# Kernel optimization log

Measured on AMD Instinct MI355X. Metric: run time of the kernel, lower is better.

Reference implementation:

```python
import jax, jax.numpy as jnp
import numpy as np

N_NODES = 100000
N_EDGES = 1600000
N_REL = 8
IN_CH = 64
HIDDEN = 64
OUT_CH = 32


def setup_inputs() -> dict:
    key = jax.random.key(0)
    ks = jax.random.split(key, 10)
    s_in = 1.0 / np.sqrt(IN_CH)
    s_h = 1.0 / np.sqrt(HIDDEN)
    return {
        "x": jax.random.normal(ks[0], (N_NODES, IN_CH), dtype=jnp.float32),
        "edge_index": jax.random.randint(ks[1], (2, N_EDGES), 0, N_NODES, dtype=jnp.int64),
        "edge_type": jax.random.randint(ks[2], (N_EDGES,), 0, N_REL, dtype=jnp.int64),
        "W0": jax.random.normal(ks[3], (N_REL, IN_CH, HIDDEN), dtype=jnp.float32) * s_in,
        "Q0": jax.random.normal(ks[4], (HIDDEN, 1), dtype=jnp.float32) * s_h,
        "K0": jax.random.normal(ks[5], (HIDDEN, 1), dtype=jnp.float32) * s_h,
        "b0": jnp.zeros((HIDDEN,), dtype=jnp.float32),
        "W1": jax.random.normal(ks[6], (N_REL, HIDDEN, OUT_CH), dtype=jnp.float32) * s_h,
        "Q1": jax.random.normal(ks[7], (OUT_CH, 1), dtype=jnp.float32) * (1.0 / np.sqrt(OUT_CH)),
        "K1": jax.random.normal(ks[8], (OUT_CH, 1), dtype=jnp.float32) * (1.0 / np.sqrt(OUT_CH)),
        "b1": jnp.zeros((OUT_CH,), dtype=jnp.float32),
    }


def rgat_conv(x, src, dst, et, W, Q, K, b, n_nodes):
    # relation-typed transform of all nodes: [R, N, out]
    xw = jnp.einsum("ni,rio->rno", x, W)
    # per-node, per-relation attention logits (heads=1, dim=1)
    q = jnp.einsum("rno,od->rnd", xw, Q)[..., 0]  # [R, N]
    k = jnp.einsum("rno,od->rnd", xw, K)[..., 0]  # [R, N]
    # additive self-attention, leaky_relu slope 0.2 (PyG RGATConv default)
    alpha = jax.nn.leaky_relu(q[et, dst] + k[et, src], negative_slope=0.2)  # [E]
    # across-relation segment softmax over incoming edges of each dst node
    amax = jax.ops.segment_max(alpha, dst, num_segments=n_nodes)
    a = jnp.exp(alpha - amax[dst])
    denom = jax.ops.segment_sum(a, dst, num_segments=n_nodes)
    a = a / (denom[dst] + 1e-16)
    # weighted scatter-add aggregation of transformed source features
    msg = a[:, None] * xw[et, src]  # [E, out]
    return jax.ops.segment_sum(msg, dst, num_segments=n_nodes) + b


def reference(x, edge_index, edge_type, W0, Q0, K0, b0, W1, Q1, K1, b1):
    src, dst = edge_index[0], edge_index[1]
    n = x.shape[0]
    h = rgat_conv(x, src, dst, edge_type, W0, Q0, K0, b0, n)
    h = jax.nn.relu(h)  # dropout p=0.0 -> identity
    out = rgat_conv(h, src, dst, edge_type, W1, Q1, K1, b1, n)
    return out
```

## Files before the change

kernel.cpp:

```cpp
#include <hip/hip_runtime.h>
#include <hip/hip_bf16.h>
#include <math.h>


#define CSR_CHUNK 8192

__global__ void k_bhist(const int* __restrict__ dst, int* __restrict__ bcount,
                        int E, int NB) {
    __shared__ int h[512];
    int t = threadIdx.x;
    for (int i = t; i < NB; i += 256) h[i] = 0;
    __syncthreads();
    int e0 = blockIdx.x * CSR_CHUNK;
    int e1 = min(e0 + CSR_CHUNK, E);
    for (int i = e0 + t; i < e1; i += 256) atomicAdd(&h[dst[i] >> 8], 1);
    __syncthreads();
    for (int i = t; i < NB; i += 256) {
        int c = h[i];
        if (c) atomicAdd(&bcount[i], c);
    }
}

__global__ void k_bscan(const int* __restrict__ bcount, int* __restrict__ bstart,
                        int* __restrict__ gcur, int* __restrict__ rowptr,
                        int NB, int N, int E) {
    __shared__ int s[512];
    int t = threadIdx.x;
    int v = (t < NB) ? bcount[t] : 0;
    s[t] = v;
    __syncthreads();
    for (int off = 1; off < 512; off <<= 1) {
        int a = (t >= off) ? s[t - off] : 0;
        __syncthreads();
        s[t] += a;
        __syncthreads();
    }
    int excl = s[t] - v;
    if (t < NB) {
        bstart[t] = excl;
        gcur[t] = excl;
    }
    if (t == 0) {
        bstart[NB] = E;
        rowptr[N] = E;
    }
}

__global__ void k_bscatter(const int* __restrict__ src, const int* __restrict__ dst,
                           const int* __restrict__ et, int* __restrict__ gcur,
                           unsigned* __restrict__ ebuf, int E, int NB) {
    __shared__ int h[512];
    __shared__ int basearr[512];
    int t = threadIdx.x;
    for (int i = t; i < NB; i += 256) h[i] = 0;
    __syncthreads();
    int e0 = blockIdx.x * CSR_CHUNK;
    int e1 = min(e0 + CSR_CHUNK, E);
    for (int i = e0 + t; i < e1; i += 256) atomicAdd(&h[dst[i] >> 8], 1);
    __syncthreads();
    for (int i = t; i < NB; i += 256) {
        int c = h[i];
        basearr[i] = c ? atomicAdd(&gcur[i], c) : 0;
        h[i] = 0;
    }
    __syncthreads();
    for (int i = e0 + t; i < e1; i += 256) {
        int d = dst[i];
        int b = d >> 8;
        int off = atomicAdd(&h[b], 1);
        ebuf[basearr[b] + off] =
            ((unsigned)(d & 255) << 20) | ((unsigned)et[i] << 17) | (unsigned)src[i];
    }
}

__global__ void k_bsort(const unsigned* __restrict__ ebuf, const int* __restrict__ bstart,
                        int* __restrict__ rowptr, int* __restrict__ csr, int N) {
    __shared__ int lh[2048];
    __shared__ int ls[2048];
    __shared__ int ss[256];
    int b = blockIdx.x, t = threadIdx.x;
    int e0 = bstart[b], e1 = bstart[b + 1];
    for (int i = t; i < 2048; i += 256) lh[i] = 0;
    __syncthreads();
    for (int i = e0 + t; i < e1; i += 256) {
        unsigned u = ebuf[i];
        atomicAdd(&lh[(int)(((u >> 20) & 255) * 8 + ((u >> 17) & 7))], 1);
    }
    __syncthreads();
    int loc[8];
    int s = 0;
#pragma unroll
    for (int j = 0; j < 8; j++) {
        loc[j] = s;
        s += lh[t * 8 + j];
    }
    ss[t] = s;
    __syncthreads();
    for (int off = 1; off < 256; off <<= 1) {
        int a = (t >= off) ? ss[t - off] : 0;
        __syncthreads();
        ss[t] += a;
        __syncthreads();
    }
    int excl = ss[t] - s;
#pragma unroll
    for (int j = 0; j < 8; j++) ls[t * 8 + j] = excl + loc[j];
    int node = b * 256 + t;
    if (node < N) rowptr[node] = e0 + excl;
    __syncthreads();
    for (int i = t; i < 2048; i += 256) lh[i] = 0;
    __syncthreads();
    for (int i = e0 + t; i < e1; i += 256) {
        unsigned u = ebuf[i];
        int key = (int)(((u >> 20) & 255) * 8 + ((u >> 17) & 7));
        int off = atomicAdd(&lh[key], 1);
        csr[e0 + ls[key] + off] = (int)u;
    }
}


__global__ void k_wt2(const float* __restrict__ W, __hip_bfloat16* __restrict__ hi,
                      __hip_bfloat16* __restrict__ lo, int OUT, int total) {
    int t = blockIdx.x * blockDim.x + threadIdx.x;
    if (t < total) {
        int per = 64 * OUT;
        int r = t / per;
        int rem = t % per;
        int i = rem / OUT;
        int o = rem % OUT;
        float v = W[t];
        __hip_bfloat16 h = __float2bfloat16(v);
        __hip_bfloat16 l = __float2bfloat16(v - __bfloat162float(h));
        size_t idx = (size_t)o * 512 + i * 8 + r;
        hi[idx] = h;
        lo[idx] = l;
    }
}

__global__ void k_wqk(const float* W, const float* Qv, const float* Kv,
                      float* wq, float* wk, int OUT) {
    int t = blockIdx.x * blockDim.x + threadIdx.x;
    if (t < 8 * 64) {
        int r = t >> 6, i = t & 63;
        const float* wrow = W + ((size_t)r * 64 + i) * OUT;
        float a = 0.f, b = 0.f;
        for (int o = 0; o < OUT; o++) {
            float w = wrow[o];
            a += w * Qv[o];
            b += w * Kv[o];
        }
        wq[t] = a;
        wk[t] = b;
    }
}

__global__ __launch_bounds__(256) void k_qk2(
        const float* __restrict__ xin, const float* __restrict__ wq,
        const float* __restrict__ wk, float* __restrict__ qn,
        float* __restrict__ kn, unsigned short* __restrict__ xbb, int N) {
    __shared__ float xt[64][65];
    __shared__ float swq[8 * 65], swk[8 * 65];
    int t = threadIdx.x;
    int nb0 = blockIdx.x * 64;
    for (int i = t; i < 512; i += 256) {
        int r = i >> 6, c = i & 63;
        swq[r * 65 + c] = wq[i];
        swk[r * 65 + c] = wk[i];
    }
    for (int i = t; i < 1024; i += 256) {
        int ns = i >> 4;
        int c4 = i & 15;
        int n = nb0 + ns;
        float4 v = {0.f, 0.f, 0.f, 0.f};
        if (n < N) v = ((const float4*)xin)[(size_t)n * 16 + c4];
        xt[ns][c4 * 4 + 0] = v.x;
        xt[ns][c4 * 4 + 1] = v.y;
        xt[ns][c4 * 4 + 2] = v.z;
        xt[ns][c4 * 4 + 3] = v.w;
        if (n < N) {
            __hip_bfloat16 b0 = __float2bfloat16(v.x);
            __hip_bfloat16 b1 = __float2bfloat16(v.y);
            __hip_bfloat16 b2 = __float2bfloat16(v.z);
            __hip_bfloat16 b3 = __float2bfloat16(v.w);
            ushort4 o;
            o.x = *(unsigned short*)&b0;
            o.y = *(unsigned short*)&b1;
            o.z = *(unsigned short*)&b2;
            o.w = *(unsigned short*)&b3;
            *(ushort4*)(xbb + (size_t)n * 64 + c4 * 4) = o;
        }
    }
    __syncthreads();
#pragma unroll
    for (int g = t; g < 512; g += 256) {
        int ns = g >> 3, r = g & 7;
        int n = nb0 + ns;
        if (n < N) {
            float qa = 0.f, ka = 0.f;
#pragma unroll
            for (int i = 0; i < 64; i++) {
                float xv = xt[ns][i];
                qa += xv * swq[r * 65 + i];
                ka += xv * swk[r * 65 + i];
            }
            qn[(size_t)n * 8 + r] = qa;
            kn[(size_t)n * 8 + r] = ka;
        }
    }
}

#define ZSTR 520

#define FLUSH8()                          \
    do {                                  \
        switch (currel) {                 \
            case 0: a0 += racc; break;    \
            case 1: a1 += racc; break;    \
            case 2: a2 += racc; break;    \
            case 3: a3 += racc; break;    \
            case 4: a4 += racc; break;    \
            case 5: a5 += racc; break;    \
            case 6: a6 += racc; break;    \
            case 7: a7 += racc; break;    \
        }                                 \
    } while (0)

template <int OUT, bool RELU>
__global__ __launch_bounds__(256) void k_fused(
        const int* __restrict__ rowptr, const int* __restrict__ csr,
        const float* __restrict__ qn, const float* __restrict__ kn,
        const unsigned short* __restrict__ xb,
        const __hip_bfloat16* __restrict__ wthi,
        const __hip_bfloat16* __restrict__ wtlo,
        const float* __restrict__ bias, float* __restrict__ xout, int N) {
    using v8s = __attribute__((ext_vector_type(8))) short;
    using v4f = __attribute__((ext_vector_type(4))) float;
    __shared__ unsigned short zt[16 * ZSTR];
    int t = threadIdx.x;
    int wvu = __builtin_amdgcn_readfirstlane(t >> 6);
    int lane = t & 63;
    int nb0 = blockIdx.x * 16;

    {
        uint4 zz = {0u, 0u, 0u, 0u};
#pragma unroll
        for (int q = 0; q < 4; q++)
            *(uint4*)&zt[(wvu * 4 + q) * ZSTR + lane * 8] = zz;
    }

#pragma unroll 1
    for (int q = 0; q < 4; q++) {
        int wid = nb0 + wvu * 4 + q;
        if (wid >= N) break;
        int r0 = rowptr[wid];
        int r1 = rowptr[wid + 1];
        int qvec = 0;
        if (lane < 8) qvec = ((const int*)qn)[wid * 8 + lane];

        float a0 = 0.f, a1 = 0.f, a2 = 0.f, a3 = 0.f;
        float a4 = 0.f, a5 = 0.f, a6 = 0.f, a7 = 0.f;
        float racc = 0.f, denom = 0.f;
        int currel = 0;

#pragma unroll 1
        for (int j = r0; j < r1; j += 16) {
            int pk[16];
            float kv[16];
            unsigned short xu[16];
#pragma unroll
            for (int u = 0; u < 16; u++) {
                int ii = (j + u < r1) ? (j + u) : (r1 - 1);
                pk[u] = csr[ii];
            }
#pragma unroll
            for (int u = 0; u < 16; u++) {
                int s_ = pk[u] & 0x1FFFF;
                int r_ = (pk[u] >> 17) & 7;
                kv[u] = kn[(size_t)s_ * 8 + r_];
            }
#pragma unroll
            for (int u = 0; u < 16; u++)
                xu[u] = xb[(size_t)(pk[u] & 0x1FFFF) * 64 + lane];
#pragma unroll
            for (int u = 0; u < 16; u++) {
                int rl = (pk[u] >> 17) & 7;
                float qv = __uint_as_float(__builtin_amdgcn_readlane(qvec, rl));
                float v = qv + kv[u];
                v = fmaxf(v, 0.2f * v);
                float tv = __expf(v);
                if (j + u >= r1) tv = 0.f;
                if (rl != currel) {
                    FLUSH8();
                    currel = rl;
                    racc = 0.f;
                }
                racc += tv * __uint_as_float(((unsigned)xu[u]) << 16);
                denom += tv;
            }
        }
        FLUSH8();
        float inv = 1.f / (denom + 1e-16f);
        float av[8] = {a0, a1, a2, a3, a4, a5, a6, a7};
        unsigned short us[8];
#pragma unroll
        for (int r = 0; r < 8; r++) {
            __hip_bfloat16 b = __float2bfloat16(av[r] * inv);
            us[r] = *(unsigned short*)&b;
        }
        uint4 pack;
        pack.x = (unsigned)us[0] | ((unsigned)us[1] << 16);
        pack.y = (unsigned)us[2] | ((unsigned)us[3] << 16);
        pack.z = (unsigned)us[4] | ((unsigned)us[5] << 16);
        pack.w = (unsigned)us[6] | ((unsigned)us[7] << 16);
        *(uint4*)&zt[(wvu * 4 + q) * ZSTR + lane * 8] = pack;
    }
    __syncthreads();

    int quad = lane >> 4;
    int l15 = lane & 15;
    int nt = wvu;
    if (nt * 16 < OUT) {
        const short* wh = (const short*)wthi;
        const short* wl = (const short*)wtlo;
        v4f acc = {0.f, 0.f, 0.f, 0.f};
#pragma unroll
        for (int k0 = 0; k0 < 512; k0 += 32) {
            int koff = k0 + quad * 8;
            v8s A = *(const v8s*)&zt[l15 * ZSTR + koff];
            v8s bh = *(const v8s*)(wh + (size_t)(nt * 16 + l15) * 512 + koff);
            v8s bl = *(const v8s*)(wl + (size_t)(nt * 16 + l15) * 512 + koff);
            acc = __builtin_amdgcn_mfma_f32_16x16x32_bf16(A, bh, acc, 0, 0, 0);
            acc = __builtin_amdgcn_mfma_f32_16x16x32_bf16(A, bl, acc, 0, 0, 0);
        }
        float bcol = bias[nt * 16 + l15];
#pragma unroll
        for (int g = 0; g < 4; g++) {
            int row = nb0 + quad * 4 + g;
            if (row < N) {
                float o = acc[g] + bcol;
                if (RELU) o = fmaxf(o, 0.f);
                xout[(size_t)row * OUT + nt * 16 + l15] = o;
            }
        }
    }
}


extern "C" void kernel_launch(void* const* d_in, const int* in_sizes, int n_in,
                              void* d_out, int out_size, void* d_ws, size_t ws_size,
                              hipStream_t stream) {
    const float* x   = (const float*)d_in[0];
    const int*   ei  = (const int*)d_in[1];
    const int*   et  = (const int*)d_in[2];
    const float* W0  = (const float*)d_in[3];
    const float* Q0  = (const float*)d_in[4];
    const float* K0  = (const float*)d_in[5];
    const float* b0  = (const float*)d_in[6];
    const float* W1  = (const float*)d_in[7];
    const float* Q1  = (const float*)d_in[8];
    const float* K1  = (const float*)d_in[9];
    const float* b1  = (const float*)d_in[10];
    float* out = (float*)d_out;

    const int N = in_sizes[0] / 64;
    const int E = in_sizes[2];
    const int* src = ei;
    const int* dst = ei + E;
    const int NB = (N + 255) >> 8;

    char* p = (char*)d_ws;
    auto alloc = [&](size_t bytes) -> void* {
        void* r = (void*)p;
        p += ((bytes + 255) / 256) * 256;
        return r;
    };
    int* rowptr   = (int*)alloc((size_t)(N + 1) * 4);
    int* bcount   = (int*)alloc(513 * 4);
    int* bstart   = (int*)alloc(513 * 4);
    int* gcur     = (int*)alloc(513 * 4);
    unsigned* ebuf = (unsigned*)alloc((size_t)E * 4);
    int* csr      = (int*)alloc((size_t)E * 4);
    float* wq     = (float*)alloc(8 * 64 * 4);
    float* wk     = (float*)alloc(8 * 64 * 4);
    float* qn     = (float*)alloc((size_t)N * 8 * 4);
    float* kn     = (float*)alloc((size_t)N * 8 * 4);
    __hip_bfloat16* wthi = (__hip_bfloat16*)alloc((size_t)64 * 512 * 2);
    __hip_bfloat16* wtlo = (__hip_bfloat16*)alloc((size_t)64 * 512 * 2);
    float* h      = (float*)alloc((size_t)N * 64 * 4);
    unsigned short* xbb = (unsigned short*)alloc((size_t)N * 64 * 2);

    int nchunks = (E + CSR_CHUNK - 1) / CSR_CHUNK;
    hipMemsetAsync(bcount, 0, (size_t)NB * 4, stream);
    k_bhist<<<nchunks, 256, 0, stream>>>(dst, bcount, E, NB);
    k_bscan<<<1, 512, 0, stream>>>(bcount, bstart, gcur, rowptr, NB, N, E);
    k_bscatter<<<nchunks, 256, 0, stream>>>(src, dst, et, gcur, ebuf, E, NB);
    k_bsort<<<NB, 256, 0, stream>>>(ebuf, bstart, rowptr, csr, N);

    int nfb = (N + 15) / 16;
    int nqkb = (N + 63) / 64;

    k_wqk<<<2, 256, 0, stream>>>(W0, Q0, K0, wq, wk, 64);
    k_qk2<<<nqkb, 256, 0, stream>>>(x, wq, wk, qn, kn, xbb, N);
    k_wt2<<<(8 * 64 * 64 + 255) / 256, 256, 0, stream>>>(W0, wthi, wtlo, 64, 8 * 64 * 64);
    k_fused<64, true><<<nfb, 256, 0, stream>>>(rowptr, csr, qn, kn, xbb,
                                               wthi, wtlo, b0, h, N);

    k_wqk<<<2, 256, 0, stream>>>(W1, Q1, K1, wq, wk, 32);
    k_qk2<<<nqkb, 256, 0, stream>>>(h, wq, wk, qn, kn, xbb, N);
    k_wt2<<<(8 * 64 * 32 + 255) / 256, 256, 0, stream>>>(W1, wthi, wtlo, 32, 8 * 64 * 32);
    k_fused<32, false><<<nfb, 256, 0, stream>>>(rowptr, csr, qn, kn, xbb,
                                                wthi, wtlo, b1, out, N);
}
```

Baseline: 474.3 us.

## Pre-gather source features into dst-sorted edge message buffer via src-bucketed scatter

Adds a second bucketing of edges by source node. A new kernel reads each source node's bf16 features from shared memory and writes them into a per-edge message array laid out in dst-CSR order. A separate attention kernel computes the exp-logits and inverse denominators per dst bucket. The fused aggregation then streams messages contiguously instead of doing random gathers of source rows. This turns random reads into scattered writes of an E×64 bf16 buffer (about 200MB) plus extra sort passes, which adds a lot of memory traffic in exchange for coalesced reads.

New measurement: 484.9 us. 1.02x slower.

```diff
diff --git a/kernel.cpp b/kernel.cpp
--- a/kernel.cpp
+++ b/kernel.cpp
@@ -5,25 +5,33 @@
 
 #define CSR_CHUNK 8192
 
-__global__ void k_bhist(const int* __restrict__ dst, int* __restrict__ bcount,
+__global__ void k_bhist(const int* __restrict__ dst, const int* __restrict__ src,
+                        int* __restrict__ bcount, int* __restrict__ sbcount,
                         int E, int NB) {
     __shared__ int h[512];
-    int t = threadIdx.x;
-    for (int i = t; i < NB; i += 256) h[i] = 0;
+    __shared__ int h2[512];
+    int t = threadIdx.x;
+    for (int i = t; i < NB; i += 256) { h[i] = 0; h2[i] = 0; }
     __syncthreads();
     int e0 = blockIdx.x * CSR_CHUNK;
     int e1 = min(e0 + CSR_CHUNK, E);
-    for (int i = e0 + t; i < e1; i += 256) atomicAdd(&h[dst[i] >> 8], 1);
+    for (int i = e0 + t; i < e1; i += 256) {
+        atomicAdd(&h[dst[i] >> 8], 1);
+        atomicAdd(&h2[src[i] >> 8], 1);
+    }
     __syncthreads();
     for (int i = t; i < NB; i += 256) {
         int c = h[i];
         if (c) atomicAdd(&bcount[i], c);
+        int c2 = h2[i];
+        if (c2) atomicAdd(&sbcount[i], c2);
     }
 }
 
 __global__ void k_bscan(const int* __restrict__ bcount, int* __restrict__ bstart,
                         int* __restrict__ gcur, int* __restrict__ rowptr,
-                        int NB, int N, int E) {
+                        const int* __restrict__ sbcount, int* __restrict__ sbstart,
+                        int* __restrict__ sgcur, int NB, int N, int E) {
     __shared__ int s[512];
     int t = threadIdx.x;
     int v = (t < NB) ? bcount[t] : 0;
@@ -36,19 +44,27 @@
         __syncthreads();
     }
     int excl = s[t] - v;
-    if (t < NB) {
-        bstart[t] = excl;
-        gcur[t] = excl;
-    }
-    if (t == 0) {
-        bstart[NB] = E;
-        rowptr[N] = E;
-    }
+    if (t < NB) { bstart[t] = excl; gcur[t] = excl; }
+    if (t == 0) { bstart[NB] = E; rowptr[N] = E; }
+    __syncthreads();
+    int v2 = (t < NB) ? sbcount[t] : 0;
+    s[t] = v2;
+    __syncthreads();
+    for (int off = 1; off < 512; off <<= 1) {
+        int a = (t >= off) ? s[t - off] : 0;
+        __syncthreads();
+        s[t] += a;
+        __syncthreads();
+    }
+    int excl2 = s[t] - v2;
+    if (t < NB) { sbstart[t] = excl2; sgcur[t] = excl2; }
+    if (t == 0) sbstart[NB] = E;
 }
 
 __global__ void k_bscatter(const int* __restrict__ src, const int* __restrict__ dst,
                            const int* __restrict__ et, int* __restrict__ gcur,
-                           unsigned* __restrict__ ebuf, int E, int NB) {
+                           unsigned* __restrict__ ebufA, int* __restrict__ ebufE,
+                           int E, int NB) {
     __shared__ int h[512];
     __shared__ int basearr[512];
     int t = threadIdx.x;
@@ -68,13 +84,16 @@
         int d = dst[i];
         int b = d >> 8;
         int off = atomicAdd(&h[b], 1);
-        ebuf[basearr[b] + off] =
-            ((unsigned)(d & 255) << 20) | ((unsigned)et[i] << 17) | (unsigned)src[i];
-    }
-}
-
-__global__ void k_bsort(const unsigned* __restrict__ ebuf, const int* __restrict__ bstart,
-                        int* __restrict__ rowptr, int* __restrict__ csr, int N) {
+        int pos = basearr[b] + off;
+        ebufA[pos] = ((unsigned)(d & 255) << 20) | ((unsigned)et[i] << 17) | (unsigned)src[i];
+        ebufE[pos] = i;
+    }
+}
+
+__global__ void k_bsort(const unsigned* __restrict__ ebufA, const int* __restrict__ ebufE,
+                        const int* __restrict__ bstart, int* __restrict__ rowptr,
+                        int* __restrict__ csr_pk, unsigned short* __restrict__ csr2,
+                        int* __restrict__ eidpos, int N) {
     __shared__ int lh[2048];
     __shared__ int ls[2048];
     __shared__ int ss[256];
@@ -83,7 +102,7 @@
     for (int i = t; i < 2048; i += 256) lh[i] = 0;
     __syncthreads();
     for (int i = e0 + t; i < e1; i += 256) {
-        unsigned u = ebuf[i];
+        unsigned u = ebufA[i];
         atomicAdd(&lh[(int)(((u >> 20) & 255) * 8 + ((u >> 17) & 7))], 1);
     }
     __syncthreads();
@@ -111,10 +130,40 @@
     for (int i = t; i < 2048; i += 256) lh[i] = 0;
     __syncthreads();
     for (int i = e0 + t; i < e1; i += 256) {
-        unsigned u = ebuf[i];
+        unsigned u = ebufA[i];
         int key = (int)(((u >> 20) & 255) * 8 + ((u >> 17) & 7));
         int off = atomicAdd(&lh[key], 1);
-        csr[e0 + ls[key] + off] = (int)u;
+        int cpos = e0 + ls[key] + off;
+        csr_pk[cpos] = (int)u;
+        csr2[cpos] = (unsigned short)((((u >> 20) & 255) << 3) | ((u >> 17) & 7));
+        if (eidpos) eidpos[ebufE[i]] = cpos;
+    }
+}
+
+__global__ void k_bscatter2(const int* __restrict__ src, const int* __restrict__ et,
+                            const int* __restrict__ eidpos, int* __restrict__ sgcur,
+                            unsigned* __restrict__ srcb, int E, int NB) {
+    __shared__ int h[512];
+    __shared__ int basearr[512];
+    int t = threadIdx.x;
+    for (int i = t; i < NB; i += 256) h[i] = 0;
+    __syncthreads();
+    int e0 = blockIdx.x * CSR_CHUNK;
+    int e1 = min(e0 + CSR_CHUNK, E);
+    for (int i = e0 + t; i < e1; i += 256) atomicAdd(&h[src[i] >> 8], 1);
+    __syncthreads();
+    for (int i = t; i < NB; i += 256) {
+        int c = h[i];
+        basearr[i] = c ? atomicAdd(&sgcur[i], c) : 0;
+        h[i] = 0;
+    }
+    __syncthreads();
+    for (int i = e0 + t; i < e1; i += 256) {
+        int sv = src[i];
+        int b = sv >> 8;
+        int off = atomicAdd(&h[b], 1);
+        srcb[basearr[b] + off] = ((unsigned)(sv & 255) << 24) |
+                                 ((unsigned)et[i] << 21) | (unsigned)eidpos[i];
     }
 }
 
@@ -209,6 +258,74 @@
     }
 }
 
+__global__ __launch_bounds__(256) void k_msg(
+        const unsigned* __restrict__ srcb, const int* __restrict__ sbstart,
+        const unsigned short* __restrict__ xbb, const float* __restrict__ kn,
+        unsigned short* __restrict__ msg, float* __restrict__ kvarr, int N) {
+    __shared__ unsigned short xrow[256 * 64];
+    __shared__ float knl[256 * 8];
+    int t = threadIdx.x;
+    int wv = t >> 6;
+    int lane = t & 63;
+    int b = blockIdx.x >> 2;
+    int qq = blockIdx.x & 3;
+    int nb = b * 256;
+    for (int idx = t; idx < 8192; idx += 256) {
+        int node = nb + (idx >> 5);
+        ((unsigned*)xrow)[idx] =
+            (node < N) ? ((const unsigned*)xbb)[(size_t)node * 32 + (idx & 31)] : 0u;
+    }
+    for (int idx = t; idx < 2048; idx += 256) {
+        int node = nb + (idx >> 3);
+        knl[idx] = (node < N) ? kn[(size_t)node * 8 + (idx & 7)] : 0.f;
+    }
+    __syncthreads();
+    int sb0 = sbstart[b], sb1 = sbstart[b + 1];
+    int len = sb1 - sb0;
+    int q0 = sb0 + ((len * qq) >> 2);
+    int q1 = sb0 + ((len * (qq + 1)) >> 2);
+    for (int i = q0 + wv; i < q1; i += 4) {
+        unsigned rec = (unsigned)__builtin_amdgcn_readfirstlane((int)srcb[i]);
+        int srcl = rec >> 24;
+        int rel = (rec >> 21) & 7;
+        int cp = rec & 0x1FFFFF;
+        unsigned short xv = xrow[srcl * 64 + lane];
+        msg[(size_t)cp * 64 + lane] = xv;
+        if (lane == 0) kvarr[cp] = knl[srcl * 8 + rel];
+    }
+}
+
+__global__ __launch_bounds__(256) void k_att(
+        const unsigned short* __restrict__ csr2, const float* __restrict__ kvarr,
+        const float* __restrict__ qn, const int* __restrict__ bstart,
+        float* __restrict__ tva, float* __restrict__ invden, int N) {
+    __shared__ float sq[2048];
+    __shared__ float sden[256];
+    int t = threadIdx.x;
+    int b = blockIdx.x;
+    int nb = b * 256;
+    for (int idx = t; idx < 2048; idx += 256) {
+        int node = nb + (idx >> 3);
+        sq[idx] = (node < N) ? qn[(size_t)node * 8 + (idx & 7)] : 0.f;
+    }
+    sden[t] = 0.f;
+    __syncthreads();
+    int e0 = bstart[b], e1 = bstart[b + 1];
+    for (int e = e0 + t; e < e1; e += 256) {
+        int c2 = csr2[e];
+        int dl = c2 >> 3;
+        int rel = c2 & 7;
+        float v = sq[dl * 8 + rel] + kvarr[e];
+        v = fmaxf(v, 0.2f * v);
+        float tvv = __expf(v);
+        tva[e] = tvv;
+        atomicAdd(&sden[dl], tvv);
+    }
+    __syncthreads();
+    int node = nb + t;
+    if (node < N) invden[node] = 1.f / (sden[t] + 1e-16f);
+}
+
 #define ZSTR 520
 
 #define FLUSH8()                          \
@@ -226,6 +343,113 @@
     } while (0)
 
 template <int OUT, bool RELU>
+__global__ __launch_bounds__(256) void k_fused2(
+        const int* __restrict__ rowptr, const unsigned short* __restrict__ csr2,
+        const float* __restrict__ tva, const float* __restrict__ invden,
+        const unsigned short* __restrict__ msg,
+        const __hip_bfloat16* __restrict__ wthi,
+        const __hip_bfloat16* __restrict__ wtlo,
+        const float* __restrict__ bias, float* __restrict__ xout, int N) {
+    using v8s = __attribute__((ext_vector_type(8))) short;
+    using v4f = __attribute__((ext_vector_type(4))) float;
+    __shared__ unsigned short zt[16 * ZSTR];
+    int t = threadIdx.x;
+    int wvu = __builtin_amdgcn_readfirstlane(t >> 6);
+    int lane = t & 63;
+    int nb0 = blockIdx.x * 16;
+
+    {
+        uint4 zz = {0u, 0u, 0u, 0u};
+#pragma unroll
+        for (int q = 0; q < 4; q++)
+            *(uint4*)&zt[(wvu * 4 + q) * ZSTR + lane * 8] = zz;
+    }
+
+#pragma unroll 1
+    for (int q = 0; q < 4; q++) {
+        int wid = nb0 + wvu * 4 + q;
+        if (wid >= N) break;
+        int r0 = rowptr[wid];
+        int r1 = rowptr[wid + 1];
+        float a0 = 0.f, a1 = 0.f, a2 = 0.f, a3 = 0.f;
+        float a4 = 0.f, a5 = 0.f, a6 = 0.f, a7 = 0.f;
+        float racc = 0.f;
+        int currel = 0;
+#pragma unroll 1
+        for (int j = r0; j < r1; j += 16) {
+            int c2[16];
+            float tvv[16];
+            unsigned short xu[16];
+#pragma unroll
+            for (int u = 0; u < 16; u++) {
+                int ii = (j + u < r1) ? (j + u) : (r1 - 1);
+                c2[u] = csr2[ii];
+                tvv[u] = (j + u < r1) ? tva[ii] : 0.f;
+            }
+#pragma unroll
+            for (int u = 0; u < 16; u++) {
+                int ii = (j + u < r1) ? (j + u) : (r1 - 1);
+                xu[u] = msg[(size_t)ii * 64 + lane];
+            }
+#pragma unroll
+            for (int u = 0; u < 16; u++) {
+                int rl = c2[u] & 7;
+                if (rl != currel) {
+                    FLUSH8();
+                    currel = rl;
+                    racc = 0.f;
+                }
+                racc += tvv[u] * __uint_as_float(((unsigned)xu[u]) << 16);
+            }
+        }
+        FLUSH8();
+        float inv = invden[wid];
+        float av[8] = {a0, a1, a2, a3, a4, a5, a6, a7};
+        unsigned short us[8];
+#pragma unroll
+        for (int r = 0; r < 8; r++) {
+            __hip_bfloat16 b = __float2bfloat16(av[r] * inv);
+            us[r] = *(unsigned short*)&b;
+        }
+        uint4 pack;
+        pack.x = (unsigned)us[0] | ((unsigned)us[1] << 16);
+        pack.y = (unsigned)us[2] | ((unsigned)us[3] << 16);
+        pack.z = (unsigned)us[4] | ((unsigned)us[5] << 16);
+        pack.w = (unsigned)us[6] | ((unsigned)us[7] << 16);
+        *(uint4*)&zt[(wvu * 4 + q) * ZSTR + lane * 8] = pack;
+    }
+    __syncthreads();
+
+    int quad = lane >> 4;
+    int l15 = lane & 15;
+    int nt = wvu;
+    if (nt * 16 < OUT) {
+        const short* wh = (const short*)wthi;
+        const short* wl = (const short*)wtlo;
+        v4f acc = {0.f, 0.f, 0.f, 0.f};
+#pragma unroll
+        for (int k0 = 0; k0 < 512; k0 += 32) {
+            int koff = k0 + quad * 8;
+            v8s A = *(const v8s*)&zt[l15 * ZSTR + koff];
+            v8s bh = *(const v8s*)(wh + (size_t)(nt * 16 + l15) * 512 + koff);
+            v8s bl = *(const v8s*)(wl + (size_t)(nt * 16 + l15) * 512 + koff);
+            acc = __builtin_amdgcn_mfma_f32_16x16x32_bf16(A, bh, acc, 0, 0, 0);
+            acc = __builtin_amdgcn_mfma_f32_16x16x32_bf16(A, bl, acc, 0, 0, 0);
+        }
+        float bcol = bias[nt * 16 + l15];
+#pragma unroll
+        for (int g = 0; g < 4; g++) {
+            int row = nb0 + quad * 4 + g;
+            if (row < N) {
+                float o = acc[g] + bcol;
+                if (RELU) o = fmaxf(o, 0.f);
+                xout[(size_t)row * OUT + nt * 16 + l15] = o;
+            }
+        }
+    }
+}
+
+template <int OUT, bool RELU>
 __global__ __launch_bounds__(256) void k_fused(
         const int* __restrict__ rowptr, const int* __restrict__ csr,
         const float* __restrict__ qn, const float* __restrict__ kn,
@@ -240,14 +464,12 @@
     int wvu = __builtin_amdgcn_readfirstlane(t >> 6);
     int lane = t & 63;
     int nb0 = blockIdx.x * 16;
-
     {
         uint4 zz = {0u, 0u, 0u, 0u};
 #pragma unroll
         for (int q = 0; q < 4; q++)
             *(uint4*)&zt[(wvu * 4 + q) * ZSTR + lane * 8] = zz;
     }
-
 #pragma unroll 1
     for (int q = 0; q < 4; q++) {
         int wid = nb0 + wvu * 4 + q;
@@ -256,12 +478,10 @@
         int r1 = rowptr[wid + 1];
         int qvec = 0;
         if (lane < 8) qvec = ((const int*)qn)[wid * 8 + lane];
-
         float a0 = 0.f, a1 = 0.f, a2 = 0.f, a3 = 0.f;
         float a4 = 0.f, a5 = 0.f, a6 = 0.f, a7 = 0.f;
         float racc = 0.f, denom = 0.f;
         int currel = 0;
-
 #pragma unroll 1
         for (int j = r0; j < r1; j += 16) {
             int pk[16];
@@ -315,7 +535,6 @@
         *(uint4*)&zt[(wvu * 4 + q) * ZSTR + lane * 8] = pack;
     }
     __syncthreads();
-
     int quad = lane >> 4;
     int l15 = lane & 15;
     int nt = wvu;
@@ -376,10 +595,15 @@
     };
     int* rowptr   = (int*)alloc((size_t)(N + 1) * 4);
     int* bcount   = (int*)alloc(513 * 4);
+    int* gcur     = (int*)alloc(513 * 4);
+    int* sbcount  = (int*)alloc(513 * 4);
+    int* sgcur    = (int*)alloc(513 * 4);
     int* bstart   = (int*)alloc(513 * 4);
-    int* gcur     = (int*)alloc(513 * 4);
-    unsigned* ebuf = (unsigned*)alloc((size_t)E * 4);
-    int* csr      = (int*)alloc((size_t)E * 4);
+    int* sbstart  = (int*)alloc(513 * 4);
+    unsigned* ebufA = (unsigned*)alloc((size_t)E * 4);
+    int* ebufE    = (int*)alloc((size_t)E * 4);
+    int* csr_pk   = (int*)alloc((size_t)E * 4);
+    unsigned short* csr2 = (unsigned short*)alloc((size_t)E * 2);
     float* wq     = (float*)alloc(8 * 64 * 4);
     float* wk     = (float*)alloc(8 * 64 * 4);
     float* qn     = (float*)alloc((size_t)N * 8 * 4);
@@ -388,13 +612,26 @@
     __hip_bfloat16* wtlo = (__hip_bfloat16*)alloc((size_t)64 * 512 * 2);
     float* h      = (float*)alloc((size_t)N * 64 * 4);
     unsigned short* xbb = (unsigned short*)alloc((size_t)N * 64 * 2);
+    int* eidpos   = (int*)alloc((size_t)E * 4);
+    unsigned* srcb = (unsigned*)alloc((size_t)E * 4);
+    float* tva    = (float*)alloc((size_t)E * 4);
+    float* kvarr  = (float*)alloc((size_t)E * 4);
+    float* invden = (float*)alloc((size_t)N * 4);
+    unsigned short* msg = (unsigned short*)alloc((size_t)E * 64 * 2);
+
+    size_t need = (size_t)(p - (char*)d_ws);
+    bool newok = (need <= ws_size) && (E < (1 << 21)) && (NB <= 512);
 
     int nchunks = (E + CSR_CHUNK - 1) / CSR_CHUNK;
-    hipMemsetAsync(bcount, 0, (size_t)NB * 4, stream);
-    k_bhist<<<nchunks, 256, 0, stream>>>(dst, bcount, E, NB);
-    k_bscan<<<1, 512, 0, stream>>>(bcount, bstart, gcur, rowptr, NB, N, E);
-    k_bscatter<<<nchunks, 256, 0, stream>>>(src, dst, et, gcur, ebuf, E, NB);
-    k_bsort<<<NB, 256, 0, stream>>>(ebuf, bstart, rowptr, csr, N);
+    hipMemsetAsync(bcount, 0, 4 * 2304, stream);
+    k_bhist<<<nchunks, 256, 0, stream>>>(dst, src, bcount, sbcount, E, NB);
+    k_bscan<<<1, 512, 0, stream>>>(bcount, bstart, gcur, rowptr,
+                                   sbcount, sbstart, sgcur, NB, N, E);
+    k_bscatter<<<nchunks, 256, 0, stream>>>(src, dst, et, gcur, ebufA, ebufE, E, NB);
+    k_bsort<<<NB, 256, 0, stream>>>(ebufA, ebufE, bstart, rowptr, csr_pk, csr2,
+                                    newok ? eidpos : (int*)nullptr, N);
+    if (newok)
+        k_bscatter2<<<nchunks, 256, 0, stream>>>(src, et, eidpos, sgcur, srcb, E, NB);
 
     int nfb = (N + 15) / 16;
     int nqkb = (N + 63) / 64;
@@ -402,12 +639,26 @@
     k_wqk<<<2, 256, 0, stream>>>(W0, Q0, K0, wq, wk, 64);
     k_qk2<<<nqkb, 256, 0, stream>>>(x, wq, wk, qn, kn, xbb, N);
     k_wt2<<<(8 * 64 * 64 + 255) / 256, 256, 0, stream>>>(W0, wthi, wtlo, 64, 8 * 64 * 64);
-    k_fused<64, true><<<nfb, 256, 0, stream>>>(rowptr, csr, qn, kn, xbb,
-                                               wthi, wtlo, b0, h, N);
+    if (newok) {
+        k_msg<<<NB * 4, 256, 0, stream>>>(srcb, sbstart, xbb, kn, msg, kvarr, N);
+        k_att<<<NB, 256, 0, stream>>>(csr2, kvarr, qn, bstart, tva, invden, N);
+        k_fused2<64, true><<<nfb, 256, 0, stream>>>(rowptr, csr2, tva, invden, msg,
+                                                    wthi, wtlo, b0, h, N);
+    } else {
+        k_fused<64, true><<<nfb, 256, 0, stream>>>(rowptr, csr_pk, qn, kn, xbb,
+                                                   wthi, wtlo, b0, h, N);
+    }
 
     k_wqk<<<2, 256, 0, stream>>>(W1, Q1, K1, wq, wk, 32);
     k_qk2<<<nqkb, 256, 0, stream>>>(h, wq, wk, qn, kn, xbb, N);
     k_wt2<<<(8 * 64 * 32 + 255) / 256, 256, 0, stream>>>(W1, wthi, wtlo, 32, 8 * 64 * 32);
-    k_fused<32, false><<<nfb, 256, 0, stream>>>(rowptr, csr, qn, kn, xbb,
-                                                wthi, wtlo, b1, out, N);
-}
+    if (newok) {
+        k_msg<<<NB * 4, 256, 0, stream>>>(srcb, sbstart, xbb, kn, msg, kvarr, N);
+        k_att<<<NB, 256, 0, stream>>>(csr2, kvarr, qn, bstart, tva, invden, N);
+        k_fused2<32, false><<<nfb, 256, 0, stream>>>(rowptr, csr2, tva, invden, msg,
+                                                     wthi, wtlo, b1, out, N);
+    } else {
+        k_fused<32, false><<<nfb, 256, 0, stream>>>(rowptr, csr_pk, qn, kn, xbb,
+                                                    wthi, wtlo, b1, out, N);
+    }
+}
```

## Bucket CSR edges by source window and sweep windows across a wave's nodes

Applied to the files above, without the earlier changes.

The CSR build now sorts each destination's edges by source-id window (source >> 14, 7 windows) and then by relation, and emits per-node window row pointers. The fused aggregation kernel loops over windows on the outside and over the wave's 4 nodes inside. Gathers of kn and xb issued close together then fall in the same source range, which is meant to improve cache locality. In exchange, the edge batch shrinks from 16 to 4 and each node's roughly 16 edges split into many short per-window segments. That means more partially filled batches, less memory-level parallelism, more relation flushes and higher register pressure from the 4x8 accumulators.

Result: slower. 649.8 us (+37.0%).

```diff
diff --git a/kernel.cpp b/kernel.cpp
--- a/kernel.cpp
+++ b/kernel.cpp
@@ -4,6 +4,8 @@
 
 
 #define CSR_CHUNK 8192
+#define NWIN 7
+#define BINS (256 * NWIN * 8)
 
 __global__ void k_bhist(const int* __restrict__ dst, int* __restrict__ bcount,
                         int E, int NB) {
@@ -22,8 +24,7 @@
 }
 
 __global__ void k_bscan(const int* __restrict__ bcount, int* __restrict__ bstart,
-                        int* __restrict__ gcur, int* __restrict__ rowptr,
-                        int NB, int N, int E) {
+                        int* __restrict__ gcur, int NB, int E) {
     __shared__ int s[512];
     int t = threadIdx.x;
     int v = (t < NB) ? bcount[t] : 0;
@@ -40,10 +41,7 @@
         bstart[t] = excl;
         gcur[t] = excl;
     }
-    if (t == 0) {
-        bstart[NB] = E;
-        rowptr[N] = E;
-    }
+    if (t == 0) bstart[NB] = E;
 }
 
 __global__ void k_bscatter(const int* __restrict__ src, const int* __restrict__ dst,
@@ -74,25 +72,27 @@
 }
 
 __global__ void k_bsort(const unsigned* __restrict__ ebuf, const int* __restrict__ bstart,
-                        int* __restrict__ rowptr, int* __restrict__ csr, int N) {
-    __shared__ int lh[2048];
-    __shared__ int ls[2048];
+                        int* __restrict__ rp2, int* __restrict__ csr, int N) {
+    __shared__ int lh[BINS];
     __shared__ int ss[256];
     int b = blockIdx.x, t = threadIdx.x;
     int e0 = bstart[b], e1 = bstart[b + 1];
-    for (int i = t; i < 2048; i += 256) lh[i] = 0;
+    for (int i = t; i < BINS; i += 256) lh[i] = 0;
     __syncthreads();
     for (int i = e0 + t; i < e1; i += 256) {
         unsigned u = ebuf[i];
-        atomicAdd(&lh[(int)(((u >> 20) & 255) * 8 + ((u >> 17) & 7))], 1);
-    }
-    __syncthreads();
-    int loc[8];
+        int dl = (u >> 20) & 255;
+        int rel = (u >> 17) & 7;
+        int w = min((int)(u & 0x1FFFF) >> 14, NWIN - 1);
+        atomicAdd(&lh[dl * (NWIN * 8) + w * 8 + rel], 1);
+    }
+    __syncthreads();
     int s = 0;
-#pragma unroll
-    for (int j = 0; j < 8; j++) {
-        loc[j] = s;
-        s += lh[t * 8 + j];
+#pragma unroll 1
+    for (int k = 0; k < NWIN * 8; k++) {
+        int c = lh[t * (NWIN * 8) + k];
+        lh[t * (NWIN * 8) + k] = s;
+        s += c;
     }
     ss[t] = s;
     __syncthreads();
@@ -103,18 +103,24 @@
         __syncthreads();
     }
     int excl = ss[t] - s;
-#pragma unroll
-    for (int j = 0; j < 8; j++) ls[t * 8 + j] = excl + loc[j];
+#pragma unroll 1
+    for (int k = 0; k < NWIN * 8; k++) lh[t * (NWIN * 8) + k] += excl;
+    __syncthreads();
     int node = b * 256 + t;
-    if (node < N) rowptr[node] = e0 + excl;
-    __syncthreads();
-    for (int i = t; i < 2048; i += 256) lh[i] = 0;
+    if (node < N) {
+#pragma unroll
+        for (int p = 0; p < NWIN; p++)
+            rp2[node * 8 + p] = e0 + lh[t * (NWIN * 8) + p * 8];
+        rp2[node * 8 + 7] = (t < 255) ? (e0 + lh[(t + 1) * (NWIN * 8)]) : e1;
+    }
     __syncthreads();
     for (int i = e0 + t; i < e1; i += 256) {
         unsigned u = ebuf[i];
-        int key = (int)(((u >> 20) & 255) * 8 + ((u >> 17) & 7));
-        int off = atomicAdd(&lh[key], 1);
-        csr[e0 + ls[key] + off] = (int)u;
+        int dl = (u >> 20) & 255;
+        int rel = (u >> 17) & 7;
+        int w = min((int)(u & 0x1FFFF) >> 14, NWIN - 1);
+        int pos = e0 + atomicAdd(&lh[dl * (NWIN * 8) + w * 8 + rel], 1);
+        csr[pos] = (int)(u & 0xFFFFF);
     }
 }
 
@@ -211,23 +217,23 @@
 
 #define ZSTR 520
 
-#define FLUSH8()                          \
-    do {                                  \
-        switch (currel) {                 \
-            case 0: a0 += racc; break;    \
-            case 1: a1 += racc; break;    \
-            case 2: a2 += racc; break;    \
-            case 3: a3 += racc; break;    \
-            case 4: a4 += racc; break;    \
-            case 5: a5 += racc; break;    \
-            case 6: a6 += racc; break;    \
-            case 7: a7 += racc; break;    \
-        }                                 \
+#define FLUSHQ(Q)                                   \
+    do {                                            \
+        switch (currel[Q]) {                        \
+            case 0: acc[Q][0] += racc[Q]; break;    \
+            case 1: acc[Q][1] += racc[Q]; break;    \
+            case 2: acc[Q][2] += racc[Q]; break;    \
+            case 3: acc[Q][3] += racc[Q]; break;    \
+            case 4: acc[Q][4] += racc[Q]; break;    \
+            case 5: acc[Q][5] += racc[Q]; break;    \
+            case 6: acc[Q][6] += racc[Q]; break;    \
+            case 7: acc[Q][7] += racc[Q]; break;    \
+        }                                           \
     } while (0)
 
 template <int OUT, bool RELU>
 __global__ __launch_bounds__(256) void k_fused(
-        const int* __restrict__ rowptr, const int* __restrict__ csr,
+        const int* __restrict__ rp2, const int* __restrict__ csr,
         const float* __restrict__ qn, const float* __restrict__ kn,
         const unsigned short* __restrict__ xb,
         const __hip_bfloat16* __restrict__ wthi,
@@ -248,71 +254,89 @@
             *(uint4*)&zt[(wvu * 4 + q) * ZSTR + lane * 8] = zz;
     }
 
+    float acc[4][8];
+    float racc[4], denom[4];
+    int currel[4], qvec[4];
+#pragma unroll
+    for (int q = 0; q < 4; q++) {
+#pragma unroll
+        for (int r = 0; r < 8; r++) acc[q][r] = 0.f;
+        racc[q] = 0.f;
+        denom[q] = 0.f;
+        currel[q] = 0;
+        int nq = nb0 + wvu * 4 + q;
+        qvec[q] = 0;
+        if (nq < N && lane < 8) qvec[q] = ((const int*)qn)[nq * 8 + lane];
+    }
+
 #pragma unroll 1
+    for (int p = 0; p < NWIN; p++) {
+#pragma unroll
+        for (int q = 0; q < 4; q++) {
+            int nq = nb0 + wvu * 4 + q;
+            if (nq < N) {
+                int r0 = rp2[nq * 8 + p];
+                int r1 = rp2[nq * 8 + p + 1];
+#pragma unroll 1
+                for (int j = r0; j < r1; j += 4) {
+                    int pk[4];
+                    float kv[4];
+                    unsigned short xu[4];
+#pragma unroll
+                    for (int u = 0; u < 4; u++) {
+                        int ii = (j + u < r1) ? (j + u) : (r1 - 1);
+                        pk[u] = csr[ii];
+                    }
+#pragma unroll
+                    for (int u = 0; u < 4; u++) {
+                        int s_ = pk[u] & 0x1FFFF;
+                        int r_ = (pk[u] >> 17) & 7;
+                        kv[u] = kn[(size_t)s_ * 8 + r_];
+                    }
+#pragma unroll
+                    for (int u = 0; u < 4; u++)
+                        xu[u] = xb[(size_t)(pk[u] & 0x1FFFF) * 64 + lane];
+#pragma unroll
+                    for (int u = 0; u < 4; u++) {
+                        int rl = (pk[u] >> 17) & 7;
+                        float qv = __uint_as_float(
+                            __builtin_amdgcn_readlane(qvec[q], rl));
+                        float v = qv + kv[u];
+                        v = fmaxf(v, 0.2f * v);
+                        float tv = __expf(v);
+                        if (j + u >= r1) tv = 0.f;
+                        if (rl != currel[q]) {
+                            FLUSHQ(q);
+                            currel[q] = rl;
+                            racc[q] = 0.f;
+                        }
+                        racc[q] += tv * __uint_as_float(((unsigned)xu[u]) << 16);
+                        denom[q] += tv;
+                    }
+                }
+            }
+        }
+    }
+
+#pragma unroll
     for (int q = 0; q < 4; q++) {
-        int wid = nb0 + wvu * 4 + q;
-        if (wid >= N) break;
-        int r0 = rowptr[wid];
-        int r1 = rowptr[wid + 1];
-        int qvec = 0;
-        if (lane < 8) qvec = ((const int*)qn)[wid * 8 + lane];
-
-        float a0 = 0.f, a1 = 0.f, a2 = 0.f, a3 = 0.f;
-        float a4 = 0.f, a5 = 0.f, a6 = 0.f, a7 = 0.f;
-        float racc = 0.f, denom = 0.f;
-        int currel = 0;
-
-#pragma unroll 1
-        for (int j = r0; j < r1; j += 16) {
-            int pk[16];
-            float kv[16];
-            unsigned short xu[16];
-#pragma unroll
-            for (int u = 0; u < 16; u++) {
-                int ii = (j + u < r1) ? (j + u) : (r1 - 1);
-                pk[u] = csr[ii];
+        int nq = nb0 + wvu * 4 + q;
+        if (nq < N) {
+            FLUSHQ(q);
+            float inv = 1.f / (denom[q] + 1e-16f);
+            unsigned short us[8];
+#pragma unroll
+            for (int r = 0; r < 8; r++) {
+                __hip_bfloat16 b = __float2bfloat16(acc[q][r] * inv);
+                us[r] = *(unsigned short*)&b;
             }
-#pragma unroll
-            for (int u = 0; u < 16; u++) {
-                int s_ = pk[u] & 0x1FFFF;
-                int r_ = (pk[u] >> 17) & 7;
-                kv[u] = kn[(size_t)s_ * 8 + r_];
-            }
-#pragma unroll
-            for (int u = 0; u < 16; u++)
-                xu[u] = xb[(size_t)(pk[u] & 0x1FFFF) * 64 + lane];
-#pragma unroll
-            for (int u = 0; u < 16; u++) {
-                int rl = (pk[u] >> 17) & 7;
-                float qv = __uint_as_float(__builtin_amdgcn_readlane(qvec, rl));
-                float v = qv + kv[u];
-                v = fmaxf(v, 0.2f * v);
-                float tv = __expf(v);
-                if (j + u >= r1) tv = 0.f;
-                if (rl != currel) {
-                    FLUSH8();
-                    currel = rl;
-                    racc = 0.f;
-                }
-                racc += tv * __uint_as_float(((unsigned)xu[u]) << 16);
-                denom += tv;
-            }
-        }
-        FLUSH8();
-        float inv = 1.f / (denom + 1e-16f);
-        float av[8] = {a0, a1, a2, a3, a4, a5, a6, a7};
-        unsigned short us[8];
-#pragma unroll
-        for (int r = 0; r < 8; r++) {
-            __hip_bfloat16 b = __float2bfloat16(av[r] * inv);
-            us[r] = *(unsigned short*)&b;
-        }
-        uint4 pack;
-        pack.x = (unsigned)us[0] | ((unsigned)us[1] << 16);
-        pack.y = (unsigned)us[2] | ((unsigned)us[3] << 16);
-        pack.z = (unsigned)us[4] | ((unsigned)us[5] << 16);
-        pack.w = (unsigned)us[6] | ((unsigned)us[7] << 16);
-        *(uint4*)&zt[(wvu * 4 + q) * ZSTR + lane * 8] = pack;
+            uint4 pack;
+            pack.x = (unsigned)us[0] | ((unsigned)us[1] << 16);
+            pack.y = (unsigned)us[2] | ((unsigned)us[3] << 16);
+            pack.z = (unsigned)us[4] | ((unsigned)us[5] << 16);
+            pack.w = (unsigned)us[6] | ((unsigned)us[7] << 16);
+            *(uint4*)&zt[(wvu * 4 + q) * ZSTR + lane * 8] = pack;
+        }
     }
     __syncthreads();
 
@@ -322,22 +346,22 @@
     if (nt * 16 < OUT) {
         const short* wh = (const short*)wthi;
         const short* wl = (const short*)wtlo;
-        v4f acc = {0.f, 0.f, 0.f, 0.f};
+        v4f acc2 = {0.f, 0.f, 0.f, 0.f};
 #pragma unroll
         for (int k0 = 0; k0 < 512; k0 += 32) {
             int koff = k0 + quad * 8;
             v8s A = *(const v8s*)&zt[l15 * ZSTR + koff];
             v8s bh = *(const v8s*)(wh + (size_t)(nt * 16 + l15) * 512 + koff);
             v8s bl = *(const v8s*)(wl + (size_t)(nt * 16 + l15) * 512 + koff);
-            acc = __builtin_amdgcn_mfma_f32_16x16x32_bf16(A, bh, acc, 0, 0, 0);
-            acc = __builtin_amdgcn_mfma_f32_16x16x32_bf16(A, bl, acc, 0, 0, 0);
+            acc2 = __builtin_amdgcn_mfma_f32_16x16x32_bf16(A, bh, acc2, 0, 0, 0);
+            acc2 = __builtin_amdgcn_mfma_f32_16x16x32_bf16(A, bl, acc2, 0, 0, 0);
         }
         float bcol = bias[nt * 16 + l15];
 #pragma unroll
         for (int g = 0; g < 4; g++) {
             int row = nb0 + quad * 4 + g;
             if (row < N) {
-                float o = acc[g] + bcol;
+                float o = acc2[g] + bcol;
                 if (RELU) o = fmaxf(o, 0.f);
                 xout[(size_t)row * OUT + nt * 16 + l15] = o;
             }
@@ -374,7 +398,7 @@
         p += ((bytes + 255) / 256) * 256;
         return r;
     };
-    int* rowptr   = (int*)alloc((size_t)(N + 1) * 4);
+    int* rp2      = (int*)alloc((size_t)N * 8 * 4);
     int* bcount   = (int*)alloc(513 * 4);
     int* bstart   = (int*)alloc(513 * 4);
     int* gcur     = (int*)alloc(513 * 4);
@@ -392,9 +416,9 @@
     int nchunks = (E + CSR_CHUNK - 1) / CSR_CHUNK;
     hipMemsetAsync(bcount, 0, (size_t)NB * 4, stream);
     k_bhist<<<nchunks, 256, 0, stream>>>(dst, bcount, E, NB);
-    k_bscan<<<1, 512, 0, stream>>>(bcount, bstart, gcur, rowptr, NB, N, E);
+    k_bscan<<<1, 512, 0, stream>>>(bcount, bstart, gcur, NB, E);
     k_bscatter<<<nchunks, 256, 0, stream>>>(src, dst, et, gcur, ebuf, E, NB);
-    k_bsort<<<NB, 256, 0, stream>>>(ebuf, bstart, rowptr, csr, N);
+    k_bsort<<<NB, 256, 0, stream>>>(ebuf, bstart, rp2, csr, N);
 
     int nfb = (N + 15) / 16;
     int nqkb = (N + 63) / 64;
@@ -402,12 +426,12 @@
     k_wqk<<<2, 256, 0, stream>>>(W0, Q0, K0, wq, wk, 64);
     k_qk2<<<nqkb, 256, 0, stream>>>(x, wq, wk, qn, kn, xbb, N);
     k_wt2<<<(8 * 64 * 64 + 255) / 256, 256, 0, stream>>>(W0, wthi, wtlo, 64, 8 * 64 * 64);
-    k_fused<64, true><<<nfb, 256, 0, stream>>>(rowptr, csr, qn, kn, xbb,
+    k_fused<64, true><<<nfb, 256, 0, stream>>>(rp2, csr, qn, kn, xbb,
                                                wthi, wtlo, b0, h, N);
 
     k_wqk<<<2, 256, 0, stream>>>(W1, Q1, K1, wq, wk, 32);
     k_qk2<<<nqkb, 256, 0, stream>>>(h, wq, wk, qn, kn, xbb, N);
     k_wt2<<<(8 * 64 * 32 + 255) / 256, 256, 0, stream>>>(W1, wthi, wtlo, 32, 8 * 64 * 32);
-    k_fused<32, false><<<nfb, 256, 0, stream>>>(rowptr, csr, qn, kn, xbb,
+    k_fused<32, false><<<nfb, 256, 0, stream>>>(rp2, csr, qn, kn, xbb,
                                                 wthi, wtlo, b1, out, N);
 }
```
